# Performance work log

Measured on AMD Instinct MI355X. Metric: run time of the kernel, lower is better.

## Reference

```python
import jax, jax.numpy as jnp
import numpy as np

G, T, H, E, F, C = 8, 2048, 512, 8, 2048, 256


def setup_inputs() -> dict:
    key = jax.random.key(0)
    ks = jax.random.split(key, 4)
    s = 0.02  # truncated-normal stddev in the original init (plain normal here)
    return {
        "x": jax.random.normal(ks[0], (G, T, H), jnp.float32),
        "router_kernel": jax.random.normal(ks[1], (H, E), jnp.float32) * s,
        "router_bias": jnp.zeros((E,), jnp.float32),
        "wi": jax.random.normal(ks[2], (E, H, F), jnp.float32) * s,
        "bi": jnp.zeros((E, F), jnp.float32),
        "wo": jax.random.normal(ks[3], (E, F, H), jnp.float32) * s,
        "bo": jnp.zeros((E, H), jnp.float32),
        "expert_capacity": C,
    }


def reference(x, router_kernel, router_bias, wi, bi, wo, bo, expert_capacity):
    # ---- Router (eval mode: no jitter noise, no dropout) ----
    # logits / probs: [g, t, e]
    router_logits = jnp.einsum("gth,he->gte", x, router_kernel) + router_bias
    router_probs = jax.nn.softmax(router_logits, axis=-1)

    # Experts-choose masked routing: each expert picks its top-capacity tokens.
    probs_et = jnp.swapaxes(router_probs, 1, 2)              # [g, e, t]
    expert_gate, expert_index = jax.lax.top_k(probs_et, expert_capacity)  # [g, e, c]
    dispatch = jax.nn.one_hot(expert_index, x.shape[1], dtype=x.dtype)    # [g, e, c, t]
    combine = dispatch * expert_gate[..., None]                            # [g, e, c, t]

    # ---- Dispatch: gather tokens into per-expert buffers ----
    expert_inputs = jnp.einsum("gect,gth->gech", dispatch, x)  # [g, e, c, h]

    # ---- Per-expert FFN (batched einsum GEMMs) ----
    h_mid = jax.nn.gelu(
        jnp.einsum("gech,ehf->gecf", expert_inputs, wi) + bi[None, :, None, :],
        approximate=False,
    )
    expert_out = jnp.einsum("gecf,efh->gech", h_mid, wo) + bo[None, :, None, :]

    # ---- Combine: scatter expert outputs back, scaled by router prob ----
    y = jnp.einsum("gect,gech->gth", combine, expert_out)  # [g, t, h]
    return y
```

## Files before the change

### kernel.cpp

```cpp
#include <hip/hip_runtime.h>
#include <cstdint>
#include <cstddef>

#define G_ 8
#define T_ 2048
#define H_ 512
#define E_ 8
#define F_ 2048
#define C_ 256

typedef __bf16 bf16x8 __attribute__((ext_vector_type(8)));
typedef float f32x4 __attribute__((ext_vector_type(4)));

__device__ __forceinline__ unsigned short f2bf(float f) {
  unsigned u = __float_as_uint(f);
  u += 0x7FFFu + ((u >> 16) & 1u);
  return (unsigned short)(u >> 16);
}

__device__ __forceinline__ void gload_lds16(const void* g, void* l) {
  __builtin_amdgcn_global_load_lds(
      (const __attribute__((address_space(1))) void*)g,
      (__attribute__((address_space(3))) void*)l, 16, 0, 0);
}

__device__ __forceinline__ float fast_gelu(float v) {
  float z = v * (1.5957691216f + 0.0713540727f * v * v);
  float e = __expf(-z);
  return v * __builtin_amdgcn_rcpf(1.0f + e);
}

#define BARRIER() do { __builtin_amdgcn_s_barrier(); asm volatile("" ::: "memory"); } while (0)

__device__ __forceinline__ void transconv_body(const float* __restrict__ in,
                                               unsigned short* __restrict__ out,
                                               int R, int Cc, int tC, int bidrem,
                                               float* smem) {
  int tid = threadIdx.x;
  int nT = (R / 64) * tC;
  int b = bidrem / nT;
  int rem = bidrem % nT;
  int tr = rem / tC, tc = rem % tC;
  const float* ib = in + (size_t)b * R * Cc + (size_t)(tr * 64) * Cc + tc * 64;
  unsigned short* ob = out + (size_t)b * R * Cc;
  int lr = tid >> 4, lc = (tid & 15) * 4;
#pragma unroll
  for (int i = 0; i < 4; ++i) {
    float4 v = *(const float4*)&ib[(size_t)(lr + 16 * i) * Cc + lc];
    smem[(lr + 16 * i) * 65 + lc + 0] = v.x;
    smem[(lr + 16 * i) * 65 + lc + 1] = v.y;
    smem[(lr + 16 * i) * 65 + lc + 2] = v.z;
    smem[(lr + 16 * i) * 65 + lc + 3] = v.w;
  }
  __syncthreads();
  int r = (tid & 31) * 2, c0 = tid >> 5;
#pragma unroll
  for (int i = 0; i < 8; ++i) {
    int c = c0 + i * 8;
    ushort2 o;
    o.x = f2bf(smem[r * 65 + c]);
    o.y = f2bf(smem[(r + 1) * 65 + c]);
    *(ushort2*)&ob[(size_t)(tc * 64 + c) * R + tr * 64 + r] = o;
  }
}

__device__ __forceinline__ void router_body(const float* __restrict__ x,
                                            const float* __restrict__ rk,
                                            const float* __restrict__ rb,
                                            float* __restrict__ probs,
                                            int bidrem, float* rks) {
  int tid = threadIdx.x;
  for (int i = tid; i < H_ * E_ / 4; i += 256)
    ((float4*)rks)[i] = ((const float4*)rk)[i];
  __syncthreads();
  int wid = tid >> 6, lane = tid & 63;
  int row = bidrem * 4 + wid;
  float acc[E_];
#pragma unroll
  for (int e = 0; e < E_; ++e) acc[e] = 0.f;
  const float* xr = x + (size_t)row * H_;
#pragma unroll
  for (int j = 0; j < H_ / 64; ++j) {
    int h = j * 64 + lane;
    float xv = xr[h];
    const float4* r4 = (const float4*)&rks[h * E_];
    float4 r0 = r4[0], r1 = r4[1];
    acc[0] += xv * r0.x; acc[1] += xv * r0.y; acc[2] += xv * r0.z; acc[3] += xv * r0.w;
    acc[4] += xv * r1.x; acc[5] += xv * r1.y; acc[6] += xv * r1.z; acc[7] += xv * r1.w;
  }
#pragma unroll
  for (int e = 0; e < E_; ++e) {
#pragma unroll
    for (int off = 32; off > 0; off >>= 1) acc[e] += __shfl_xor(acc[e], off);
  }
  float l[E_];
  float mx = -1e30f;
#pragma unroll
  for (int e = 0; e < E_; ++e) { l[e] = acc[e] + rb[e]; mx = fmaxf(mx, l[e]); }
  float s = 0.f;
#pragma unroll
  for (int e = 0; e < E_; ++e) { l[e] = expf(l[e] - mx); s += l[e]; }
  float inv = 1.0f / s;
  int g = row >> 11, t = row & (T_ - 1);
  if (lane < E_) probs[((size_t)(g * E_ + lane)) * T_ + t] = l[lane] * inv;
}

__global__ __launch_bounds__(256) void fused1_kernel(const float* __restrict__ wi,
                                                     unsigned short* __restrict__ wiT,
                                                     const float* __restrict__ wo,
                                                     unsigned short* __restrict__ woT,
                                                     const float* __restrict__ x,
                                                     const float* __restrict__ rk,
                                                     const float* __restrict__ rb,
                                                     float* __restrict__ probs) {
  __shared__ float smem[64 * 65];
  int bid = blockIdx.x;
  if (bid < 2048) {
    transconv_body(wi, wiT, H_, F_, F_ / 64, bid, smem);
  } else if (bid < 4096) {
    transconv_body(wo, woT, F_, H_, H_ / 64, bid - 2048, smem);
  } else {
    router_body(x, rk, rb, probs, bid - 4096, smem);
  }
}

__global__ __launch_bounds__(1024) void topk_kernel(const float* __restrict__ probs,
                                                    int* __restrict__ idx,
                                                    float* __restrict__ gate) {
  __shared__ unsigned long long keys[T_];
  int ge = blockIdx.x, tid = threadIdx.x;
  const float* p = probs + (size_t)ge * T_;
#pragma unroll
  for (int j = 0; j < 2; ++j) {
    int t = tid + j * 1024;
    unsigned pb = __float_as_uint(p[t]);
    keys[t] = ((unsigned long long)pb << 32) | (unsigned)(~t);
  }
  __syncthreads();
  for (unsigned k = 2; k <= T_; k <<= 1) {
    for (unsigned j = k >> 1; j > 0; j >>= 1) {
      unsigned w = tid;
      unsigned i = ((w & ~(j - 1)) << 1) | (w & (j - 1));
      unsigned q = i + j;
      unsigned long long a = keys[i], b = keys[q];
      bool sw = ((i & k) == 0) ? (a < b) : (a > b);
      if (sw) { keys[i] = b; keys[q] = a; }
      __syncthreads();
    }
  }
  if (tid < C_) {
    unsigned long long kk = keys[tid];
    gate[ge * C_ + tid] = __uint_as_float((unsigned)(kk >> 32));
    idx[ge * C_ + tid] = (int)(~(unsigned)kk);
  }
}

__global__ __launch_bounds__(256) void fused2_kernel(const float* __restrict__ x,
                                                     const int* __restrict__ idx,
                                                     unsigned short* __restrict__ xin,
                                                     int* __restrict__ cnt,
                                                     unsigned short* __restrict__ ent) {
  int bid = blockIdx.x, tid = threadIdx.x;
  if (bid < 4096) {
    int wid = tid >> 6, lane = tid & 63;
    int r = bid * 4 + wid;
    int ge = r >> 8;
    int g = ge >> 3;
    int t = idx[r];
    const float* src = x + ((size_t)(g * T_ + t)) * H_;
    unsigned short* dst = xin + (size_t)r * H_;
#pragma unroll
    for (int j = 0; j < 2; ++j) {
      int h = j * 256 + lane * 4;
      float4 v = *(const float4*)&src[h];
      ushort4 o;
      o.x = f2bf(v.x); o.y = f2bf(v.y); o.z = f2bf(v.z); o.w = f2bf(v.w);
      *(ushort4*)&dst[h] = o;
    }
  } else {
    int id = (bid - 4096) * 256 + tid;
    int ge = id >> 8, c = id & 255;
    int g = ge >> 3, e = ge & 7;
    int t = idx[id];
    int pos = atomicAdd(&cnt[g * T_ + t], 1);
    ent[(g * T_ + t) * 8 + pos] = (unsigned short)((e << 8) | c);
  }
}

__global__ __launch_bounds__(256) void combine_kernel(const unsigned short* __restrict__ eout,
                                                      const int* __restrict__ cnt,
                                                      const unsigned short* __restrict__ ent,
                                                      const float* __restrict__ gate,
                                                      float* __restrict__ y) {
  int tid = threadIdx.x, wid = tid >> 6, lane = tid & 63;
  int row = blockIdx.x * 4 + wid;
  int g = row >> 11;
  int n = cnt[row];
  float a[8] = {0.f, 0.f, 0.f, 0.f, 0.f, 0.f, 0.f, 0.f};
  for (int i = 0; i < n; ++i) {
    unsigned pe = ent[row * 8 + i];
    int e = pe >> 8, c = pe & 255;
    int ge = g * E_ + e;
    float gv = gate[ge * C_ + c];
    bf16x8 v = *(const bf16x8*)&eout[((size_t)ge * C_ + c) * H_ + lane * 8];
#pragma unroll
    for (int j = 0; j < 8; ++j) a[j] += gv * (float)v[j];
  }
  float* yr = y + (size_t)row * H_ + lane * 8;
  *(float4*)yr = make_float4(a[0], a[1], a[2], a[3]);
  *(float4*)(yr + 4) = make_float4(a[4], a[5], a[6], a[7]);
}

template<int NT>
__device__ __forceinline__ void gemm_core(const unsigned short* __restrict__ Abase,
                                          const unsigned short* __restrict__ Bbase,
                                          int ldK, unsigned short* lds,
                                          f32x4 (&acc)[8][4]) {
  int tid = threadIdx.x;
  int wid = tid >> 6, lane = tid & 63;
  int l15 = lane & 15, g4 = lane >> 4;
  int wm = wid >> 2, wn = wid & 3;

  int off0, off1;
  {
    int ob = tid * 16;
    int lr = ob >> 7, b = ((ob >> 4) & 7) ^ (lr & 7);
    off0 = (2 * lr + (b >> 2)) * ldK + (b & 3) * 8;
    ob = 8192 + tid * 16;
    lr = ob >> 7; b = ((ob >> 4) & 7) ^ (lr & 7);
    off1 = (2 * lr + (b >> 2)) * ldK + (b & 3) * 8;
  }
  int blkphys = (((l15 & 1) << 2) | g4) ^ (l15 >> 1);
  int abase = (wm * 64 + (l15 >> 1)) * 64 + blkphys * 8;
  int bbase = 8192 + (wn * 32 + (l15 >> 1)) * 64 + blkphys * 8;

  auto stage = [&](int kt) {
    unsigned short* sb = lds + (kt & 3) * 16384;
    const unsigned short* ga = Abase + kt * 32;
    const unsigned short* gb = Bbase + kt * 32;
    gload_lds16(ga + off0, sb + wid * 512);
    gload_lds16(ga + off1, sb + 4096 + wid * 512);
    gload_lds16(gb + off0, sb + 8192 + wid * 512);
    gload_lds16(gb + off1, sb + 12288 + wid * 512);
  };

  auto compute = [&](int kt) {
    const unsigned short* sb = lds + (kt & 3) * 16384;
    bf16x8 af[8], bfr[4];
#pragma unroll
    for (int m = 0; m < 8; ++m) af[m] = *(const bf16x8*)&sb[abase + m * 512];
#pragma unroll
    for (int n = 0; n < 4; ++n) bfr[n] = *(const bf16x8*)&sb[bbase + n * 512];
    __builtin_amdgcn_s_setprio(1);
#pragma unroll
    for (int m = 0; m < 8; ++m)
#pragma unroll
      for (int n = 0; n < 4; ++n)
        acc[m][n] = __builtin_amdgcn_mfma_f32_16x16x32_bf16(af[m], bfr[n], acc[m][n], 0, 0, 0);
    __builtin_amdgcn_s_setprio(0);
  };

  stage(0); stage(1); stage(2);
  asm volatile("s_waitcnt vmcnt(8)" ::: "memory");
  BARRIER();
  for (int kt = 0; kt < NT - 3; ++kt) {
    stage(kt + 3);
    compute(kt);
    asm volatile("s_waitcnt vmcnt(8)" ::: "memory");
    BARRIER();
  }
  compute(NT - 3);
  asm volatile("s_waitcnt vmcnt(4)" ::: "memory");
  BARRIER();
  compute(NT - 2);
  asm volatile("s_waitcnt vmcnt(0)" ::: "memory");
  BARRIER();
  compute(NT - 1);
}

__global__ __launch_bounds__(512, 2) void gemm1_kernel(const unsigned short* __restrict__ xin,
                                                       const unsigned short* __restrict__ wiT,
                                                       const float* __restrict__ bi,
                                                       unsigned short* __restrict__ hmid) {
  __shared__ unsigned short lds[65536];
  int bid = blockIdx.x;
  int swz = (bid & 7) * 64 + (bid >> 3);
  int e = swz >> 6, rem = swz & 63, nt = rem >> 3, g = rem & 7;
  int ge = g * E_ + e;
  const unsigned short* Abase = xin + (size_t)ge * C_ * H_;
  const unsigned short* Bbase = wiT + (size_t)e * F_ * H_ + (size_t)(nt * 256) * H_;
  f32x4 acc[8][4] = {};
  gemm_core<H_ / 32>(Abase, Bbase, H_, lds, acc);

  int tid = threadIdx.x, wid = tid >> 6, lane = tid & 63;
  int l15 = lane & 15, g4 = lane >> 4, wm = wid >> 2, wn = wid & 3;
  unsigned short* Cb = hmid + (size_t)ge * C_ * F_;
  int row0 = wm * 128, col0 = nt * 256 + wn * 64;
#pragma unroll
  for (int m = 0; m < 8; ++m) {
#pragma unroll
    for (int n = 0; n < 4; ++n) {
      int col = col0 + n * 16 + l15;
      float bv = bi[e * F_ + col];
#pragma unroll
      for (int r = 0; r < 4; ++r) {
        int row = row0 + m * 16 + g4 * 4 + r;
        Cb[(size_t)row * F_ + col] = f2bf(fast_gelu(acc[m][n][r] + bv));
      }
    }
  }
}

template<int NT>
__device__ __forceinline__ void gemm2_core(const unsigned short* __restrict__ Abase,
                                           const unsigned short* __restrict__ Bbase,
                                           int ldK, unsigned short* lds,
                                           f32x4 (&acc)[4][4]) {
  int tid = threadIdx.x;
  int wid = tid >> 6, lane = tid & 63;
  int l15 = lane & 15, g4 = lane >> 4;
  int wm = wid >> 1, wn = wid & 1;

  auto mkoff = [&](int ob) {
    int lr = ob >> 7, b = ((ob >> 4) & 7) ^ (lr & 7);
    return (2 * lr + (b >> 2)) * ldK + (b & 3) * 8;
  };
  int off0 = mkoff(tid * 16);
  int off1 = mkoff(4096 + tid * 16);

  int blkphys = (((l15 & 1) << 2) | g4) ^ (l15 >> 1);
  int abase = (wm * 32 + (l15 >> 1)) * 64 + blkphys * 8;
  int bbase = 4096 + (wn * 32 + (l15 >> 1)) * 64 + blkphys * 8;

  auto stage = [&](int kt) {
    unsigned short* sb = lds + (kt & 3) * 8192;
    const unsigned short* ga = Abase + kt * 32;
    const unsigned short* gb = Bbase + kt * 32;
    gload_lds16(ga + off0, sb + wid * 512);
    gload_lds16(ga + off1, sb + 2048 + wid * 512);
    gload_lds16(gb + off0, sb + 4096 + wid * 512);
    gload_lds16(gb + off1, sb + 6144 + wid * 512);
  };

  auto compute = [&](int kt) {
    const unsigned short* sb = lds + (kt & 3) * 8192;
    bf16x8 af[4], bfr[4];
#pragma unroll
    for (int m = 0; m < 4; ++m) af[m] = *(const bf16x8*)&sb[abase + m * 512];
#pragma unroll
    for (int n = 0; n < 4; ++n) bfr[n] = *(const bf16x8*)&sb[bbase + n * 512];
    __builtin_amdgcn_s_setprio(1);
#pragma unroll
    for (int m = 0; m < 4; ++m)
#pragma unroll
      for (int n = 0; n < 4; ++n)
        acc[m][n] = __builtin_amdgcn_mfma_f32_16x16x32_bf16(af[m], bfr[n], acc[m][n], 0, 0, 0);
    __builtin_amdgcn_s_setprio(0);
  };

  stage(0); stage(1); stage(2);
  asm volatile("s_waitcnt vmcnt(8)" ::: "memory");
  BARRIER();
  for (int kt = 0; kt < NT - 3; ++kt) {
    stage(kt + 3);
    compute(kt);
    asm volatile("s_waitcnt vmcnt(8)" ::: "memory");
    BARRIER();
  }
  compute(NT - 3);
  asm volatile("s_waitcnt vmcnt(4)" ::: "memory");
  BARRIER();
  compute(NT - 2);
  asm volatile("s_waitcnt vmcnt(0)" ::: "memory");
  BARRIER();
  compute(NT - 1);
}

__global__ __launch_bounds__(256, 2) void gemm2_kernel(const unsigned short* __restrict__ hmid,
                                                       const unsigned short* __restrict__ woT,
                                                       const float* __restrict__ bo,
                                                       unsigned short* __restrict__ eout) {
  __shared__ unsigned short lds[32768];
  int bid = blockIdx.x;
  int swz = (bid & 7) * 64 + (bid >> 3);
  int e = swz >> 6, rem = swz & 63;
  int tile = rem >> 3, g = rem & 7;
  int tm = tile >> 2, tn = tile & 3;
  int ge = g * E_ + e;
  const unsigned short* Abase = hmid + (size_t)ge * C_ * F_ + (size_t)(tm * 128) * F_;
  const unsigned short* Bbase = woT + (size_t)e * H_ * F_ + (size_t)(tn * 128) * F_;
  f32x4 acc[4][4] = {};
  gemm2_core<F_ / 32>(Abase, Bbase, F_, lds, acc);

  int tid = threadIdx.x, wid = tid >> 6, lane = tid & 63;
  int l15 = lane & 15, g4 = lane >> 4, wm = wid >> 1, wn = wid & 1;
  unsigned short* Ob = eout + (size_t)ge * C_ * H_;
  int row0 = tm * 128 + wm * 64, col0 = tn * 128 + wn * 64;
#pragma unroll
  for (int m = 0; m < 4; ++m) {
#pragma unroll
    for (int n = 0; n < 4; ++n) {
      int col = col0 + n * 16 + l15;
      float bv = bo[e * H_ + col];
#pragma unroll
      for (int r = 0; r < 4; ++r) {
        int row = row0 + m * 16 + g4 * 4 + r;
        Ob[(size_t)row * H_ + col] = f2bf(acc[m][n][r] + bv);
      }
    }
  }
}

extern "C" void kernel_launch(void* const* d_in, const int* in_sizes, int n_in,
                              void* d_out, int out_size, void* d_ws, size_t ws_size,
                              hipStream_t stream) {
  const float* x  = (const float*)d_in[0];
  const float* rk = (const float*)d_in[1];
  const float* rb = (const float*)d_in[2];
  const float* wi = (const float*)d_in[3];
  const float* bi = (const float*)d_in[4];
  const float* wo = (const float*)d_in[5];
  const float* bo = (const float*)d_in[6];
  float* y = (float*)d_out;

  const size_t WI_T = 0;
  const size_t WO_T = 16777216;
  const size_t PROB = 33554432;
  const size_t IDXO = 34078720;
  const size_t GATO = 34144256;
  const size_t XINO = 34209792;
  const size_t HMID = 50987008;
  const size_t NEED = 118095872;
  if (ws_size < NEED) return;

  char* ws = (char*)d_ws;
  unsigned short* wiT = (unsigned short*)(ws + WI_T);
  unsigned short* woT = (unsigned short*)(ws + WO_T);
  float* probs = (float*)(ws + PROB);
  int* cnt = (int*)(ws + PROB);
  unsigned short* ent = (unsigned short*)(ws + PROB + 65536);
  int* idx = (int*)(ws + IDXO);
  float* gate = (float*)(ws + GATO);
  unsigned short* xin = (unsigned short*)(ws + XINO);
  unsigned short* eout = (unsigned short*)(ws + XINO);
  unsigned short* hmid = (unsigned short*)(ws + HMID);

  fused1_kernel<<<8192, 256, 0, stream>>>(wi, wiT, wo, woT, x, rk, rb, probs);
  topk_kernel<<<G_ * E_, 1024, 0, stream>>>(probs, idx, gate);
  hipMemsetAsync(cnt, 0, G_ * T_ * sizeof(int), stream);
  fused2_kernel<<<4096 + 64, 256, 0, stream>>>(x, idx, xin, cnt, ent);
  gemm1_kernel<<<512, 512, 0, stream>>>(xin, wiT, bi, hmid);
  gemm2_kernel<<<512, 256, 0, stream>>>(hmid, woT, bo, eout);
  combine_kernel<<<G_ * T_ / 4, 256, 0, stream>>>(eout, cnt, ent, gate, y);
}
```

Measured before the change: 164.5 us.

## Retile gemm1 to 128x128 blocks, fold memset and routing-table build into earlier kernels

The cnt memset moves into the fused1 kernel as 16 extra blocks, and the atomic routing-table (cnt/ent) build moves from the gather kernel into the top-k epilogue. Both remove launches and a separate memset. gemm1 drops its 256x256, 512-thread tile and reuses gemm2's 128x128, 256-thread core, giving 2048 blocks instead of 512 for better load balance across CUs. The cost is lower per-block data reuse in gemm1 and serialized atomics in top-k's tail.

```diff
diff --git a/kernel.cpp b/kernel.cpp
--- a/kernel.cpp
+++ b/kernel.cpp
@@ -112,21 +112,27 @@
                                                      const float* __restrict__ x,
                                                      const float* __restrict__ rk,
                                                      const float* __restrict__ rb,
-                                                     float* __restrict__ probs) {
+                                                     float* __restrict__ probs,
+                                                     int* __restrict__ cnt) {
   __shared__ float smem[64 * 65];
   int bid = blockIdx.x;
   if (bid < 2048) {
     transconv_body(wi, wiT, H_, F_, F_ / 64, bid, smem);
   } else if (bid < 4096) {
     transconv_body(wo, woT, F_, H_, H_ / 64, bid - 2048, smem);
+  } else if (bid < 8192) {
+    router_body(x, rk, rb, probs, bid - 4096, smem);
   } else {
-    router_body(x, rk, rb, probs, bid - 4096, smem);
+    int id = (bid - 8192) * 256 + threadIdx.x;
+    ((int4*)cnt)[id] = make_int4(0, 0, 0, 0);
   }
 }
 
 __global__ __launch_bounds__(1024) void topk_kernel(const float* __restrict__ probs,
                                                     int* __restrict__ idx,
-                                                    float* __restrict__ gate) {
+                                                    float* __restrict__ gate,
+                                                    int* __restrict__ cnt,
+                                                    unsigned short* __restrict__ ent) {
   __shared__ unsigned long long keys[T_];
   int ge = blockIdx.x, tid = threadIdx.x;
   const float* p = probs + (size_t)ge * T_;
@@ -151,39 +157,31 @@
   if (tid < C_) {
     unsigned long long kk = keys[tid];
     gate[ge * C_ + tid] = __uint_as_float((unsigned)(kk >> 32));
-    idx[ge * C_ + tid] = (int)(~(unsigned)kk);
-  }
-}
-
-__global__ __launch_bounds__(256) void fused2_kernel(const float* __restrict__ x,
+    int t = (int)(~(unsigned)kk);
+    idx[ge * C_ + tid] = t;
+    int g = ge >> 3, e = ge & 7;
+    int pos = atomicAdd(&cnt[g * T_ + t], 1);
+    ent[(g * T_ + t) * 8 + pos] = (unsigned short)((e << 8) | tid);
+  }
+}
+
+__global__ __launch_bounds__(256) void gather_kernel(const float* __restrict__ x,
                                                      const int* __restrict__ idx,
-                                                     unsigned short* __restrict__ xin,
-                                                     int* __restrict__ cnt,
-                                                     unsigned short* __restrict__ ent) {
-  int bid = blockIdx.x, tid = threadIdx.x;
-  if (bid < 4096) {
-    int wid = tid >> 6, lane = tid & 63;
-    int r = bid * 4 + wid;
-    int ge = r >> 8;
-    int g = ge >> 3;
-    int t = idx[r];
-    const float* src = x + ((size_t)(g * T_ + t)) * H_;
-    unsigned short* dst = xin + (size_t)r * H_;
-#pragma unroll
-    for (int j = 0; j < 2; ++j) {
-      int h = j * 256 + lane * 4;
-      float4 v = *(const float4*)&src[h];
-      ushort4 o;
-      o.x = f2bf(v.x); o.y = f2bf(v.y); o.z = f2bf(v.z); o.w = f2bf(v.w);
-      *(ushort4*)&dst[h] = o;
-    }
-  } else {
-    int id = (bid - 4096) * 256 + tid;
-    int ge = id >> 8, c = id & 255;
-    int g = ge >> 3, e = ge & 7;
-    int t = idx[id];
-    int pos = atomicAdd(&cnt[g * T_ + t], 1);
-    ent[(g * T_ + t) * 8 + pos] = (unsigned short)((e << 8) | c);
+                                                     unsigned short* __restrict__ xin) {
+  int tid = threadIdx.x, wid = tid >> 6, lane = tid & 63;
+  int r = blockIdx.x * 4 + wid;
+  int ge = r >> 8;
+  int g = ge >> 3;
+  int t = idx[r];
+  const float* src = x + ((size_t)(g * T_ + t)) * H_;
+  unsigned short* dst = xin + (size_t)r * H_;
+#pragma unroll
+  for (int j = 0; j < 2; ++j) {
+    int h = j * 256 + lane * 4;
+    float4 v = *(const float4*)&src[h];
+    ushort4 o;
+    o.x = f2bf(v.x); o.y = f2bf(v.y); o.z = f2bf(v.z); o.w = f2bf(v.w);
+    *(ushort4*)&dst[h] = o;
   }
 }
 
@@ -212,110 +210,10 @@
 }
 
 template<int NT>
-__device__ __forceinline__ void gemm_core(const unsigned short* __restrict__ Abase,
-                                          const unsigned short* __restrict__ Bbase,
-                                          int ldK, unsigned short* lds,
-                                          f32x4 (&acc)[8][4]) {
-  int tid = threadIdx.x;
-  int wid = tid >> 6, lane = tid & 63;
-  int l15 = lane & 15, g4 = lane >> 4;
-  int wm = wid >> 2, wn = wid & 3;
-
-  int off0, off1;
-  {
-    int ob = tid * 16;
-    int lr = ob >> 7, b = ((ob >> 4) & 7) ^ (lr & 7);
-    off0 = (2 * lr + (b >> 2)) * ldK + (b & 3) * 8;
-    ob = 8192 + tid * 16;
-    lr = ob >> 7; b = ((ob >> 4) & 7) ^ (lr & 7);
-    off1 = (2 * lr + (b >> 2)) * ldK + (b & 3) * 8;
-  }
-  int blkphys = (((l15 & 1) << 2) | g4) ^ (l15 >> 1);
-  int abase = (wm * 64 + (l15 >> 1)) * 64 + blkphys * 8;
-  int bbase = 8192 + (wn * 32 + (l15 >> 1)) * 64 + blkphys * 8;
-
-  auto stage = [&](int kt) {
-    unsigned short* sb = lds + (kt & 3) * 16384;
-    const unsigned short* ga = Abase + kt * 32;
-    const unsigned short* gb = Bbase + kt * 32;
-    gload_lds16(ga + off0, sb + wid * 512);
-    gload_lds16(ga + off1, sb + 4096 + wid * 512);
-    gload_lds16(gb + off0, sb + 8192 + wid * 512);
-    gload_lds16(gb + off1, sb + 12288 + wid * 512);
-  };
-
-  auto compute = [&](int kt) {
-    const unsigned short* sb = lds + (kt & 3) * 16384;
-    bf16x8 af[8], bfr[4];
-#pragma unroll
-    for (int m = 0; m < 8; ++m) af[m] = *(const bf16x8*)&sb[abase + m * 512];
-#pragma unroll
-    for (int n = 0; n < 4; ++n) bfr[n] = *(const bf16x8*)&sb[bbase + n * 512];
-    __builtin_amdgcn_s_setprio(1);
-#pragma unroll
-    for (int m = 0; m < 8; ++m)
-#pragma unroll
-      for (int n = 0; n < 4; ++n)
-        acc[m][n] = __builtin_amdgcn_mfma_f32_16x16x32_bf16(af[m], bfr[n], acc[m][n], 0, 0, 0);
-    __builtin_amdgcn_s_setprio(0);
-  };
-
-  stage(0); stage(1); stage(2);
-  asm volatile("s_waitcnt vmcnt(8)" ::: "memory");
-  BARRIER();
-  for (int kt = 0; kt < NT - 3; ++kt) {
-    stage(kt + 3);
-    compute(kt);
-    asm volatile("s_waitcnt vmcnt(8)" ::: "memory");
-    BARRIER();
-  }
-  compute(NT - 3);
-  asm volatile("s_waitcnt vmcnt(4)" ::: "memory");
-  BARRIER();
-  compute(NT - 2);
-  asm volatile("s_waitcnt vmcnt(0)" ::: "memory");
-  BARRIER();
-  compute(NT - 1);
-}
-
-__global__ __launch_bounds__(512, 2) void gemm1_kernel(const unsigned short* __restrict__ xin,
-                                                       const unsigned short* __restrict__ wiT,
-                                                       const float* __restrict__ bi,
-                                                       unsigned short* __restrict__ hmid) {
-  __shared__ unsigned short lds[65536];
-  int bid = blockIdx.x;
-  int swz = (bid & 7) * 64 + (bid >> 3);
-  int e = swz >> 6, rem = swz & 63, nt = rem >> 3, g = rem & 7;
-  int ge = g * E_ + e;
-  const unsigned short* Abase = xin + (size_t)ge * C_ * H_;
-  const unsigned short* Bbase = wiT + (size_t)e * F_ * H_ + (size_t)(nt * 256) * H_;
-  f32x4 acc[8][4] = {};
-  gemm_core<H_ / 32>(Abase, Bbase, H_, lds, acc);
-
-  int tid = threadIdx.x, wid = tid >> 6, lane = tid & 63;
-  int l15 = lane & 15, g4 = lane >> 4, wm = wid >> 2, wn = wid & 3;
-  unsigned short* Cb = hmid + (size_t)ge * C_ * F_;
-  int row0 = wm * 128, col0 = nt * 256 + wn * 64;
-#pragma unroll
-  for (int m = 0; m < 8; ++m) {
-#pragma unroll
-    for (int n = 0; n < 4; ++n) {
-      int col = col0 + n * 16 + l15;
-      float bv = bi[e * F_ + col];
-#pragma unroll
-      for (int r = 0; r < 4; ++r) {
-        int row = row0 + m * 16 + g4 * 4 + r;
-        Cb[(size_t)row * F_ + col] = f2bf(fast_gelu(acc[m][n][r] + bv));
-      }
-    }
-  }
-}
-
-template<int NT>
-__device__ __forceinline__ void gemm2_core(const unsigned short* __restrict__ Abase,
-                                           const unsigned short* __restrict__ Bbase,
-                                           int ldK, unsigned short* lds,
-                                           f32x4 (&acc)[4][4]) {
+__device__ __forceinline__ void gemm_core128(const unsigned short* __restrict__ Abase,
+                                             const unsigned short* __restrict__ Bbase,
+                                             int ldK, unsigned short* lds,
+                                             f32x4 (&acc)[4][4]) {
   int tid = threadIdx.x;
   int wid = tid >> 6, lane = tid & 63;
   int l15 = lane & 15, g4 = lane >> 4;
@@ -374,6 +272,40 @@
   asm volatile("s_waitcnt vmcnt(0)" ::: "memory");
   BARRIER();
   compute(NT - 1);
+}
+
+__global__ __launch_bounds__(256, 2) void gemm1_kernel(const unsigned short* __restrict__ xin,
+                                                       const unsigned short* __restrict__ wiT,
+                                                       const float* __restrict__ bi,
+                                                       unsigned short* __restrict__ hmid) {
+  __shared__ unsigned short lds[32768];
+  int bid = blockIdx.x;
+  int id = (bid & 7) * 256 + (bid >> 3);
+  int e = id >> 8, rem = id & 255;
+  int tm = rem >> 7, tn = (rem >> 3) & 15, g = rem & 7;
+  int ge = g * E_ + e;
+  const unsigned short* Abase = xin + (size_t)ge * C_ * H_ + (size_t)(tm * 128) * H_;
+  const unsigned short* Bbase = wiT + (size_t)e * F_ * H_ + (size_t)(tn * 128) * H_;
+  f32x4 acc[4][4] = {};
+  gemm_core128<H_ / 32>(Abase, Bbase, H_, lds, acc);
+
+  int tid = threadIdx.x, wid = tid >> 6, lane = tid & 63;
+  int l15 = lane & 15, g4 = lane >> 4, wm = wid >> 1, wn = wid & 1;
+  unsigned short* Cb = hmid + (size_t)ge * C_ * F_;
+  int row0 = tm * 128 + wm * 64, col0 = tn * 128 + wn * 64;
+#pragma unroll
+  for (int m = 0; m < 4; ++m) {
+#pragma unroll
+    for (int n = 0; n < 4; ++n) {
+      int col = col0 + n * 16 + l15;
+      float bv = bi[e * F_ + col];
+#pragma unroll
+      for (int r = 0; r < 4; ++r) {
+        int row = row0 + m * 16 + g4 * 4 + r;
+        Cb[(size_t)row * F_ + col] = f2bf(fast_gelu(acc[m][n][r] + bv));
+      }
+    }
+  }
 }
 
 __global__ __launch_bounds__(256, 2) void gemm2_kernel(const unsigned short* __restrict__ hmid,
@@ -390,7 +322,7 @@
   const unsigned short* Abase = hmid + (size_t)ge * C_ * F_ + (size_t)(tm * 128) * F_;
   const unsigned short* Bbase = woT + (size_t)e * H_ * F_ + (size_t)(tn * 128) * F_;
   f32x4 acc[4][4] = {};
-  gemm2_core<F_ / 32>(Abase, Bbase, F_, lds, acc);
+  gemm_core128<F_ / 32>(Abase, Bbase, F_, lds, acc);
 
   int tid = threadIdx.x, wid = tid >> 6, lane = tid & 63;
   int l15 = lane & 15, g4 = lane >> 4, wm = wid >> 1, wn = wid & 1;
@@ -426,30 +358,31 @@
   const size_t WI_T = 0;
   const size_t WO_T = 16777216;
   const size_t PROB = 33554432;
-  const size_t IDXO = 34078720;
-  const size_t GATO = 34144256;
-  const size_t XINO = 34209792;
-  const size_t HMID = 50987008;
-  const size_t NEED = 118095872;
+  const size_t CNTO = 34078720;
+  const size_t ENTO = 34144256;
+  const size_t IDXO = 34406400;
+  const size_t GATO = 34471936;
+  const size_t XINO = 34537472;
+  const size_t HMID = 51314688;
+  const size_t NEED = 118423552;
   if (ws_size < NEED) return;
 
   char* ws = (char*)d_ws;
   unsigned short* wiT = (unsigned short*)(ws + WI_T);
   unsigned short* woT = (unsigned short*)(ws + WO_T);
   float* probs = (float*)(ws + PROB);
-  int* cnt = (int*)(ws + PROB);
-  unsigned short* ent = (unsigned short*)(ws + PROB + 65536);
+  int* cnt = (int*)(ws + CNTO);
+  unsigned short* ent = (unsigned short*)(ws + ENTO);
   int* idx = (int*)(ws + IDXO);
   float* gate = (float*)(ws + GATO);
   unsigned short* xin = (unsigned short*)(ws + XINO);
   unsigned short* eout = (unsigned short*)(ws + XINO);
   unsigned short* hmid = (unsigned short*)(ws + HMID);
 
-  fused1_kernel<<<8192, 256, 0, stream>>>(wi, wiT, wo, woT, x, rk, rb, probs);
-  topk_kernel<<<G_ * E_, 1024, 0, stream>>>(probs, idx, gate);
-  hipMemsetAsync(cnt, 0, G_ * T_ * sizeof(int), stream);
-  fused2_kernel<<<4096 + 64, 256, 0, stream>>>(x, idx, xin, cnt, ent);
-  gemm1_kernel<<<512, 512, 0, stream>>>(xin, wiT, bi, hmid);
+  fused1_kernel<<<8192 + 16, 256, 0, stream>>>(wi, wiT, wo, woT, x, rk, rb, probs, cnt);
+  topk_kernel<<<G_ * E_, 1024, 0, stream>>>(probs, idx, gate, cnt, ent);
+  gather_kernel<<<G_ * E_ * C_ / 4, 256, 0, stream>>>(x, idx, xin);
+  gemm1_kernel<<<2048, 256, 0, stream>>>(xin, wiT, bi, hmid);
   gemm2_kernel<<<512, 256, 0, stream>>>(hmid, woT, bo, eout);
   combine_kernel<<<G_ * T_ / 4, 256, 0, stream>>>(eout, cnt, ent, gate, y);
 }
```

Result: faster. 155.6 us (-5.4%).
